# Optimization experiments

Measured on AMD Instinct MI355X. Metric: run time of the kernel, lower is better.

## Reference

```python
import jax, jax.numpy as jnp
import numpy as np

NUM_BEAM, NUM_NULL, NUM_BIN, NUM_CH = 8, 4, 257, 8
NUM_BLOCK, NUM_FRAME = 8, 500
ALPHA, LOW_FREQ, HIGH_FREQ = 0.35, 5, 70


def setup_inputs() -> dict:
    key = jax.random.key(0)
    k1, k2, k3, k4 = jax.random.split(key, 4)
    return {
        "input": jax.random.normal(k1, (NUM_BLOCK, NUM_FRAME, 2, NUM_BIN, NUM_CH), jnp.float32),
        "beam_id": jax.random.randint(k2, (NUM_BLOCK,), 0, NUM_BEAM),
        "targ_w": jax.random.normal(k3, (NUM_BEAM, 2, NUM_BIN, NUM_CH), jnp.float32),
        "null_w": jax.random.normal(k4, (NUM_BEAM, NUM_NULL, 2, NUM_BIN, NUM_CH), jnp.float32),
    }


def _forward(input, beam_id, targ_w, null_w):
    a = ALPHA
    xr, xi = input[:, :, 0], input[:, :, 1]            # (B,T,F,C)
    # target beamformer: select per-block complex weights (B,2,F,C)
    tw = targ_w[beam_id]
    twr, twi = tw[:, 0], tw[:, 1]                      # (B,F,C)
    tr = jnp.einsum('btfc,bfc->btf', xr, twr) - jnp.einsum('btfc,bfc->btf', xi, twi)
    ti = jnp.einsum('btfc,bfc->btf', xr, twi) + jnp.einsum('btfc,bfc->btf', xi, twr)
    tr, ti = tr[..., None], ti[..., None]              # (B,T,F,1)
    # null beamformer: (B,N,2,F,C)
    nw = null_w[beam_id]
    nwr, nwi = nw[:, :, 0], nw[:, :, 1]                # (B,N,F,C)
    nr = jnp.einsum('btfc,bnfc->btfn', xr, nwr) - jnp.einsum('btfc,bnfc->btfn', xi, nwi)
    ni = jnp.einsum('btfc,bnfc->btfn', xr, nwi) + jnp.einsum('btfc,bnfc->btfn', xi, nwr)
    # elementwise cross-spectra products (B,T,F,N)
    pr = tr * nr + ti * ni
    pi = ti * nr - tr * ni
    pw = jnp.mean(xr ** 2 + xi ** 2, axis=-1, keepdims=True)  # (B,T,F,1)

    # t = 0 (note: (1-alpha) scales only the FIRST product, as in the source)
    phi_r0 = (1.0 - a) * tr[:, 0] * nr[:, 0] + ti[:, 0] * ni[:, 0]
    phi_i0 = (1.0 - a) * ti[:, 0] * nr[:, 0] - tr[:, 0] * ni[:, 0]
    psd0 = (1.0 - a) * pw[:, 0]
    phi0 = jnp.sqrt(phi_r0 ** 2 + phi_i0 ** 2)
    dcf0 = jnp.clip(phi0 / (psd0 + 1e-13), 0.01, 1.0)

    def step(carry, xs):
        phi_r, phi_i, psd = carry
        pr_t, pi_t, pw_t = xs
        phi_r = a * phi_r + (1.0 - a) * pr_t
        phi_i = a * phi_i + (1.0 - a) * pi_t
        psd = a * psd + (1.0 - a) * pw_t
        phi = jnp.sqrt(phi_r ** 2 + phi_i ** 2)
        dcf_t = jnp.clip(phi / (psd + 1e-13), 0.01, 1.0)
        pre = jnp.sum(psd[:, LOW_FREQ:HIGH_FREQ, :], axis=1, keepdims=True)
        aft = jnp.sum(phi[:, LOW_FREQ:HIGH_FREQ, :], axis=1, keepdims=True)
        ratio = jnp.clip(aft / (pre + 1e-10), 0.01, 1.0)
        dcf_t = jnp.sqrt(dcf_t * ratio)
        return (phi_r, phi_i, psd), dcf_t

    xs = (jnp.moveaxis(pr[:, 1:], 1, 0),
          jnp.moveaxis(pi[:, 1:], 1, 0),
          jnp.moveaxis(pw[:, 1:], 1, 0))
    _, dcf_rest = jax.lax.scan(step, (phi_r0, phi_i0, psd0), xs)  # (T-1,B,F,N)
    dcf = jnp.concatenate([dcf0[None], dcf_rest], axis=0)
    dcf = jnp.moveaxis(dcf, 0, 1)                                 # (B,T,F,N)
    targ_out = jnp.stack([tr[..., 0], ti[..., 0]], axis=2)        # (B,T,2,F)
    return dcf, targ_out


def reference(input, beam_id, targ_w, null_w):
    return _forward(input, beam_id, targ_w, null_w)
```

## Files before the change

kernel.cpp:

```cpp
#include <hip/hip_runtime.h>

#define NB 8
#define NT 500
#define NF 257
#define NC 8
#define NNUL 4
#define LOWF 5
#define HIGHF 70
#define S_CHUNK 8
#define WARM 4
#define N_CHUNK 63
#define AL 0.35f

__device__ __forceinline__ float dot8(const float4& a0, const float4& a1,
                                      const float4& b0, const float4& b1) {
    return a0.x*b0.x + a0.y*b0.y + a0.z*b0.z + a0.w*b0.w
         + a1.x*b1.x + a1.y*b1.y + a1.z*b1.z + a1.w*b1.w;
}

__global__ __launch_bounds__(1024, 4) void dcf_fused_kernel(
    const float* __restrict__ x,
    const int* __restrict__ beam_id,
    const float* __restrict__ targ_w,
    const float* __restrict__ null_w,
    float* __restrict__ out)
{
    const int tid = threadIdx.x;
    const int bid = blockIdx.x;
    const int b  = bid & 7;
    const int k  = bid >> 3;
    const int t0 = k * S_CHUNK;
    const int te = min(NT, t0 + S_CHUNK);
    int ts = t0 - WARM; if (ts < 0) ts = 0;

    const int f = tid >> 2;
    const int n = tid & 3;
    const int wid = tid >> 6;
    const int lane = tid & 63;
    const bool extra = (tid < 4);

    __shared__ float s_w256[16 + 4 * 16];
    __shared__ float s_part[S_CHUNK][25];
    __shared__ float s_dcf[S_CHUNK][1028];

    const int beam = beam_id[b];
    const int pA = n & 1;
    const int offA = pA * (NF * NC);
    const int offB = (1 - pA) * (NF * NC);
    const int psel = (n == 1 || n == 2) ? 1 : 0;
    const float nsign = pA ? -1.f : 1.f;

    float4 tw0, tw1, nwA0, nwA1, nwB0, nwB1;
    {
        const float* tp = targ_w + ((size_t)(beam * 2 + psel) * NF + f) * NC;
        tw0 = *(const float4*)(tp);  tw1 = *(const float4*)(tp + 4);
        const float* qp = null_w + ((size_t)((beam * NNUL + n) * 2) * NF + f) * NC;
        nwA0 = *(const float4*)(qp + offA);  nwA1 = *(const float4*)(qp + offA + 4);
        nwB0 = *(const float4*)(qp + offB);  nwB1 = *(const float4*)(qp + offB + 4);
    }
    if (tid < 16) {
        int p = tid >> 3, c = tid & 7;
        s_w256[tid] = targ_w[((size_t)(beam * 2 + p) * NF + 256) * NC + c];
    } else if (tid < 80) {
        int i = tid - 16;
        int nn = i >> 4, p = (i >> 3) & 1, c = i & 7;
        s_w256[tid] = null_w[((size_t)((beam * NNUL + nn) * 2 + p) * NF + 256) * NC + c];
    }
    __syncthreads();

    float phi_r = 0.f, phi_i = 0.f, psd = 0.f;
    float phi_r2 = 0.f, phi_i2 = 0.f, psd2 = 0.f;
    const float a = AL, oma = 1.0f - AL;
    const size_t rowlen = 2 * NF * NC;
    const bool in_red = (f >= LOWF) && (f < HIGHF);

    const float* xrow = x + (size_t)(b * NT + ts) * rowlen + f * NC;
    float4 pA0 = *(const float4*)(xrow + offA);
    float4 pA1 = *(const float4*)(xrow + offA + 4);
    float4 pB0 = *(const float4*)(xrow + offB);
    float4 pB1 = *(const float4*)(xrow + offB + 4);

    float* outT = out + (size_t)NB * NT * NF * NNUL;

    for (int t = ts; t < te; ++t) {
        const float4 A0 = pA0, A1 = pA1, B0 = pB0, B1 = pB1;
        if (t + 1 < te) {
            const float* xr2 = x + (size_t)(b * NT + t + 1) * rowlen + f * NC;
            pA0 = *(const float4*)(xr2 + offA);
            pA1 = *(const float4*)(xr2 + offA + 4);
            pB0 = *(const float4*)(xr2 + offB);
            pB1 = *(const float4*)(xr2 + offB + 4);
        }

        const float d = dot8(A0, A1, tw0, tw1);
        const float e = __shfl_xor(d, 1);
        const float u = (n < 2) ? ((n == 0) ? (d - e) : (e - d)) : (d + e);
        const float v = __shfl_xor(u, 2);
        const float tr = (n < 2) ? u : v;
        const float ti = (n < 2) ? v : u;

        const float P = dot8(A0, A1, nwA0, nwA1);
        const float Q = dot8(B0, B1, nwB0, nwB1);
        const float nr = nsign * (P - Q);
        const float ni = dot8(A0, A1, nwB0, nwB1) + dot8(B0, B1, nwA0, nwA1);
        const float pw = (dot8(A0, A1, A0, A1) + dot8(B0, B1, B0, B1)) * 0.125f;

        if (t == 0) {
            phi_r = oma * tr * nr + ti * ni;
            phi_i = oma * ti * nr - tr * ni;
            psd   = oma * pw;
        } else {
            phi_r = a * phi_r + oma * (tr * nr + ti * ni);
            phi_i = a * phi_i + oma * (ti * nr - tr * ni);
            psd   = a * psd + oma * pw;
        }

        float tr2 = 0.f, ti2 = 0.f;
        if (extra) {
            const float* xw = x + (size_t)(b * NT + t) * rowlen + 256 * NC;
            const float4 eA0 = *(const float4*)(xw + offA);
            const float4 eA1 = *(const float4*)(xw + offA + 4);
            const float4 eB0 = *(const float4*)(xw + offB);
            const float4 eB1 = *(const float4*)(xw + offB + 4);
            const float4 etw0 = *(const float4*)&s_w256[psel * 8];
            const float4 etw1 = *(const float4*)&s_w256[psel * 8 + 4];
            const float* nq = &s_w256[16 + n * 16];
            const float4 enA0 = *(const float4*)(nq + pA * 8);
            const float4 enA1 = *(const float4*)(nq + pA * 8 + 4);
            const float4 enB0 = *(const float4*)(nq + (1 - pA) * 8);
            const float4 enB1 = *(const float4*)(nq + (1 - pA) * 8 + 4);
            const float d2 = dot8(eA0, eA1, etw0, etw1);
            const float e2 = __shfl_xor(d2, 1);
            const float u2 = (n < 2) ? ((n == 0) ? (d2 - e2) : (e2 - d2)) : (d2 + e2);
            const float v2 = __shfl_xor(u2, 2);
            tr2 = (n < 2) ? u2 : v2;
            ti2 = (n < 2) ? v2 : u2;
            const float P2 = dot8(eA0, eA1, enA0, enA1);
            const float Q2 = dot8(eB0, eB1, enB0, enB1);
            const float nr2 = nsign * (P2 - Q2);
            const float ni2 = dot8(eA0, eA1, enB0, enB1) + dot8(eB0, eB1, enA0, enA1);
            const float pw2 = (dot8(eA0, eA1, eA0, eA1) + dot8(eB0, eB1, eB0, eB1)) * 0.125f;
            if (t == 0) {
                phi_r2 = oma * tr2 * nr2 + ti2 * ni2;
                phi_i2 = oma * ti2 * nr2 - tr2 * ni2;
                psd2   = oma * pw2;
            } else {
                phi_r2 = a * phi_r2 + oma * (tr2 * nr2 + ti2 * ni2);
                phi_i2 = a * phi_i2 + oma * (ti2 * nr2 - tr2 * ni2);
                psd2   = a * psd2 + oma * pw2;
            }
        }

        if (t >= t0) {
            const int fr = t - t0;
            const float phi = sqrtf(phi_r * phi_r + phi_i * phi_i);
            const float dcfv = fminf(fmaxf(phi / (psd + 1e-13f), 0.01f), 1.0f);
            const size_t bt = (size_t)(b * NT + t);
            if (n == 0) outT[(bt * 2 + 0) * NF + f] = tr;
            if (n == 1) outT[(bt * 2 + 1) * NF + f] = ti;
            s_dcf[fr][tid] = dcfv;
            if (extra) {
                const float phi2 = sqrtf(phi_r2 * phi_r2 + phi_i2 * phi_i2);
                const float dcf2v = fminf(fmaxf(phi2 / (psd2 + 1e-13f), 0.01f), 1.0f);
                s_dcf[fr][1024 + n] = dcf2v;
                if (n == 0) outT[(bt * 2 + 0) * NF + 256] = tr2;
                if (n == 1) outT[(bt * 2 + 1) * NF + 256] = ti2;
            }
            if (wid < 5) {
                float v_phi = in_red ? phi : 0.f;
                float v_psd = (in_red && n == 0) ? psd : 0.f;
                #pragma unroll
                for (int off = 4; off < 64; off <<= 1) {
                    v_phi += __shfl_xor(v_phi, off);
                    v_psd += __shfl_xor(v_psd, off);
                }
                if (lane < 4)  s_part[fr][wid * 5 + lane] = v_phi;
                if (lane == 0) s_part[fr][wid * 5 + 4]    = v_psd;
            }
        }
    }

    __syncthreads();

    const int nf = te - t0;
    for (int fr = 0; fr < nf; ++fr) {
        const int t = t0 + fr;
        const size_t bt = (size_t)(b * NT + t);
        float dcfv = s_dcf[fr][tid];
        float dcf2v = extra ? s_dcf[fr][1024 + n] : 0.f;
        if (t >= 1) {
            const float* sp = s_part[fr];
            const float pre = sp[4] + sp[9] + sp[14] + sp[19] + sp[24];
            const float aft = sp[n] + sp[5 + n] + sp[10 + n] + sp[15 + n] + sp[20 + n];
            const float ratio = fminf(fmaxf(aft / (pre + 1e-10f), 0.01f), 1.0f);
            dcfv = sqrtf(dcfv * ratio);
            if (extra) dcf2v = sqrtf(dcf2v * ratio);
        }
        out[(bt * NF + f) * NNUL + n] = dcfv;
        if (extra) out[(bt * NF + 256) * NNUL + n] = dcf2v;
    }
}

extern "C" void kernel_launch(void* const* d_in, const int* in_sizes, int n_in,
                              void* d_out, int out_size, void* d_ws, size_t ws_size,
                              hipStream_t stream) {
    const float* x       = (const float*)d_in[0];
    const int*   beam_id = (const int*)d_in[1];
    const float* targ_w  = (const float*)d_in[2];
    const float* null_w  = (const float*)d_in[3];
    float* out           = (float*)d_out;
    (void)d_ws; (void)ws_size;

    dcf_fused_kernel<<<dim3(NB * N_CHUNK), dim3(1024), 0, stream>>>(
        x, beam_id, targ_w, null_w, out);
}
```

Measured before the change: 133.9 us.

## Use fast math intrinsics, strength-reduce addressing, and share power via shuffle

Replaces the divides, sqrt and clamps with AMDGCN rcp, sqrt and fmed3 intrinsics, and turns per-iteration index math into pointer increments. Each lane now computes only half of the channel power and combines it with a neighbour through a lane shuffle. The bin-256 work moves to the last four threads so the extra bin sits next to bin 255 in memory. Launch bounds are raised to request more occupancy. The approximate rcp and sqrt may change results slightly, and the higher occupancy target may force register spills.

```diff
diff --git a/kernel.cpp b/kernel.cpp
--- a/kernel.cpp
+++ b/kernel.cpp
@@ -12,13 +12,36 @@
 #define N_CHUNK 63
 #define AL 0.35f
 
+__device__ __forceinline__ float dot4(const float4& a, const float4& b) {
+    return a.x*b.x + a.y*b.y + a.z*b.z + a.w*b.w;
+}
 __device__ __forceinline__ float dot8(const float4& a0, const float4& a1,
                                       const float4& b0, const float4& b1) {
-    return a0.x*b0.x + a0.y*b0.y + a0.z*b0.z + a0.w*b0.w
-         + a1.x*b1.x + a1.y*b1.y + a1.z*b1.z + a1.w*b1.w;
-}
-
-__global__ __launch_bounds__(1024, 4) void dcf_fused_kernel(
+    return dot4(a0, b0) + dot4(a1, b1);
+}
+__device__ __forceinline__ float fast_rcp(float v) {
+#if __has_builtin(__builtin_amdgcn_rcpf)
+    return __builtin_amdgcn_rcpf(v);
+#else
+    return 1.0f / v;
+#endif
+}
+__device__ __forceinline__ float fast_sqrt(float v) {
+#if __has_builtin(__builtin_amdgcn_sqrtf)
+    return __builtin_amdgcn_sqrtf(v);
+#else
+    return sqrtf(v);
+#endif
+}
+__device__ __forceinline__ float clamp01(float v) {
+#if __has_builtin(__builtin_amdgcn_fmed3f)
+    return __builtin_amdgcn_fmed3f(v, 0.01f, 1.0f);
+#else
+    return fminf(fmaxf(v, 0.01f), 1.0f);
+#endif
+}
+
+__global__ __launch_bounds__(1024, 8) void dcf_fused_kernel(
     const float* __restrict__ x,
     const int* __restrict__ beam_id,
     const float* __restrict__ targ_w,
@@ -37,7 +60,7 @@
     const int n = tid & 3;
     const int wid = tid >> 6;
     const int lane = tid & 63;
-    const bool extra = (tid < 4);
+    const bool extra = (tid >= 1020);
 
     __shared__ float s_w256[16 + 4 * 16];
     __shared__ float s_part[S_CHUNK][25];
@@ -71,25 +94,29 @@
     float phi_r = 0.f, phi_i = 0.f, psd = 0.f;
     float phi_r2 = 0.f, phi_i2 = 0.f, psd2 = 0.f;
     const float a = AL, oma = 1.0f - AL;
-    const size_t rowlen = 2 * NF * NC;
+    const int rl = 2 * NF * NC;
     const bool in_red = (f >= LOWF) && (f < HIGHF);
 
-    const float* xrow = x + (size_t)(b * NT + ts) * rowlen + f * NC;
-    float4 pA0 = *(const float4*)(xrow + offA);
-    float4 pA1 = *(const float4*)(xrow + offA + 4);
-    float4 pB0 = *(const float4*)(xrow + offB);
-    float4 pB1 = *(const float4*)(xrow + offB + 4);
+    const float* xpa = x + (size_t)(b * NT + ts) * rl + f * NC + offA;
+    const float* xpb = x + (size_t)(b * NT + ts) * rl + f * NC + offB;
+    float4 pA0 = *(const float4*)(xpa);
+    float4 pA1 = *(const float4*)(xpa + 4);
+    float4 pB0 = *(const float4*)(xpb);
+    float4 pB1 = *(const float4*)(xpb + 4);
 
     float* outT = out + (size_t)NB * NT * NF * NNUL;
+    float* poT = outT + ((size_t)(b * NT + t0) * 2 + n) * NF + f;
+    float* sdp = &s_dcf[0][tid];
+    float* spp = &s_part[0][wid * 5];
 
     for (int t = ts; t < te; ++t) {
         const float4 A0 = pA0, A1 = pA1, B0 = pB0, B1 = pB1;
+        xpa += rl; xpb += rl;
         if (t + 1 < te) {
-            const float* xr2 = x + (size_t)(b * NT + t + 1) * rowlen + f * NC;
-            pA0 = *(const float4*)(xr2 + offA);
-            pA1 = *(const float4*)(xr2 + offA + 4);
-            pB0 = *(const float4*)(xr2 + offB);
-            pB1 = *(const float4*)(xr2 + offB + 4);
+            pA0 = *(const float4*)(xpa);
+            pA1 = *(const float4*)(xpa + 4);
+            pB0 = *(const float4*)(xpb);
+            pB1 = *(const float4*)(xpb + 4);
         }
 
         const float d = dot8(A0, A1, tw0, tw1);
@@ -103,7 +130,10 @@
         const float Q = dot8(B0, B1, nwB0, nwB1);
         const float nr = nsign * (P - Q);
         const float ni = dot8(A0, A1, nwB0, nwB1) + dot8(B0, B1, nwA0, nwA1);
-        const float pw = (dot8(A0, A1, A0, A1) + dot8(B0, B1, B0, B1)) * 0.125f;
+
+        float sq = dot4(A0, A0) + dot4(A1, A1);
+        sq += __shfl_xor(sq, 1);
+        const float pw = sq * 0.125f;
 
         if (t == 0) {
             phi_r = oma * tr * nr + ti * ni;
@@ -117,11 +147,12 @@
 
         float tr2 = 0.f, ti2 = 0.f;
         if (extra) {
-            const float* xw = x + (size_t)(b * NT + t) * rowlen + 256 * NC;
-            const float4 eA0 = *(const float4*)(xw + offA);
-            const float4 eA1 = *(const float4*)(xw + offA + 4);
-            const float4 eB0 = *(const float4*)(xw + offB);
-            const float4 eB1 = *(const float4*)(xw + offB + 4);
+            const float* xe  = xpa + (NC - rl);
+            const float* xe2 = xpb + (NC - rl);
+            const float4 eA0 = *(const float4*)(xe);
+            const float4 eA1 = *(const float4*)(xe + 4);
+            const float4 eB0 = *(const float4*)(xe2);
+            const float4 eB1 = *(const float4*)(xe2 + 4);
             const float4 etw0 = *(const float4*)&s_w256[psel * 8];
             const float4 etw1 = *(const float4*)&s_w256[psel * 8 + 4];
             const float* nq = &s_w256[16 + n * 16];
@@ -139,7 +170,9 @@
             const float Q2 = dot8(eB0, eB1, enB0, enB1);
             const float nr2 = nsign * (P2 - Q2);
             const float ni2 = dot8(eA0, eA1, enB0, enB1) + dot8(eB0, eB1, enA0, enA1);
-            const float pw2 = (dot8(eA0, eA1, eA0, eA1) + dot8(eB0, eB1, eB0, eB1)) * 0.125f;
+            float sq2 = dot4(eA0, eA0) + dot4(eA1, eA1);
+            sq2 += __shfl_xor(sq2, 1);
+            const float pw2 = sq2 * 0.125f;
             if (t == 0) {
                 phi_r2 = oma * tr2 * nr2 + ti2 * ni2;
                 phi_i2 = oma * ti2 * nr2 - tr2 * ni2;
@@ -152,19 +185,15 @@
         }
 
         if (t >= t0) {
-            const int fr = t - t0;
-            const float phi = sqrtf(phi_r * phi_r + phi_i * phi_i);
-            const float dcfv = fminf(fmaxf(phi / (psd + 1e-13f), 0.01f), 1.0f);
-            const size_t bt = (size_t)(b * NT + t);
-            if (n == 0) outT[(bt * 2 + 0) * NF + f] = tr;
-            if (n == 1) outT[(bt * 2 + 1) * NF + f] = ti;
-            s_dcf[fr][tid] = dcfv;
+            const float phi = fast_sqrt(phi_r * phi_r + phi_i * phi_i);
+            const float dcfv = clamp01(phi * fast_rcp(psd + 1e-13f));
+            if (n < 2) *poT = (n == 0) ? tr : ti;
+            *sdp = dcfv;
             if (extra) {
-                const float phi2 = sqrtf(phi_r2 * phi_r2 + phi_i2 * phi_i2);
-                const float dcf2v = fminf(fmaxf(phi2 / (psd2 + 1e-13f), 0.01f), 1.0f);
-                s_dcf[fr][1024 + n] = dcf2v;
-                if (n == 0) outT[(bt * 2 + 0) * NF + 256] = tr2;
-                if (n == 1) outT[(bt * 2 + 1) * NF + 256] = ti2;
+                const float phi2 = fast_sqrt(phi_r2 * phi_r2 + phi_i2 * phi_i2);
+                const float dcf2v = clamp01(phi2 * fast_rcp(psd2 + 1e-13f));
+                sdp[4] = dcf2v;
+                if (n < 2) poT[1] = (n == 0) ? tr2 : ti2;
             }
             if (wid < 5) {
                 float v_phi = in_red ? phi : 0.f;
@@ -174,30 +203,33 @@
                     v_phi += __shfl_xor(v_phi, off);
                     v_psd += __shfl_xor(v_psd, off);
                 }
-                if (lane < 4)  s_part[fr][wid * 5 + lane] = v_phi;
-                if (lane == 0) s_part[fr][wid * 5 + 4]    = v_psd;
+                if (lane < 4)  spp[lane] = v_phi;
+                if (lane == 0) spp[4]    = v_psd;
             }
+            poT += 2 * NF; sdp += 1028; spp += 25;
         }
     }
 
     __syncthreads();
 
+    float* po = out + ((size_t)(b * NT + t0) * NF + f) * NNUL + n;
+    const float* sdr = &s_dcf[0][tid];
+    const float* spr = &s_part[0][0];
     const int nf = te - t0;
     for (int fr = 0; fr < nf; ++fr) {
         const int t = t0 + fr;
-        const size_t bt = (size_t)(b * NT + t);
-        float dcfv = s_dcf[fr][tid];
-        float dcf2v = extra ? s_dcf[fr][1024 + n] : 0.f;
+        float dcfv = sdr[0];
+        float dcf2v = extra ? sdr[4] : 0.f;
         if (t >= 1) {
-            const float* sp = s_part[fr];
-            const float pre = sp[4] + sp[9] + sp[14] + sp[19] + sp[24];
-            const float aft = sp[n] + sp[5 + n] + sp[10 + n] + sp[15 + n] + sp[20 + n];
-            const float ratio = fminf(fmaxf(aft / (pre + 1e-10f), 0.01f), 1.0f);
-            dcfv = sqrtf(dcfv * ratio);
-            if (extra) dcf2v = sqrtf(dcf2v * ratio);
-        }
-        out[(bt * NF + f) * NNUL + n] = dcfv;
-        if (extra) out[(bt * NF + 256) * NNUL + n] = dcf2v;
+            const float pre = spr[4] + spr[9] + spr[14] + spr[19] + spr[24];
+            const float aft = spr[n] + spr[5 + n] + spr[10 + n] + spr[15 + n] + spr[20 + n];
+            const float ratio = clamp01(aft * fast_rcp(pre + 1e-10f));
+            dcfv = fast_sqrt(dcfv * ratio);
+            if (extra) dcf2v = fast_sqrt(dcf2v * ratio);
+        }
+        *po = dcfv;
+        if (extra) po[NNUL] = dcf2v;
+        po += NF * NNUL; sdr += 1028; spr += 25;
     }
 }
 
```

Result: slower. 382.8 us (+185.9%).
